# Performance work log

Hardware: AMD Instinct MI355X
Metric: run time of the kernel (lower is better)

The kernel has to match this reference:

```python
import jax, jax.numpy as jnp
import numpy as np

D = 512       # embed_dim
H = 8         # num_heads
HD = D // H   # head_dim = 64
B = 16
TQ = 512      # query length (current segment)
TK = 1024     # key length (memory + current)
GRU_BIAS = 2.0


def _layer_norm(x, g, b, eps=1e-5):
    mu = jnp.mean(x, axis=-1, keepdims=True)
    var = jnp.mean((x - mu) ** 2, axis=-1, keepdims=True)
    return (x - mu) * jax.lax.rsqrt(var + eps) * g + b


def _gelu(x):
    # torch nn.GELU() default is the exact erf form
    return jax.nn.gelu(x, approximate=False)


def _rel_shift(x):
    # Transformer-XL relative shift. x: [B, H, Tq, Tk]
    b, h, tq, tk = x.shape
    x = jnp.pad(x, ((0, 0), (0, 0), (0, 0), (1, 0)))
    x = x.reshape(b, h, tk + 1, tq)[:, :, 1:, :]
    return x.reshape(b, h, tq, tk)


def _gru_gate(x, y, W, bg):
    # GTrXL gating: x is the residual stream, y the sublayer output.
    Wr, Ur, Wz, Uz, Wg, Ug = W
    r = jax.nn.sigmoid(y @ Wr + x @ Ur)
    z = jax.nn.sigmoid(y @ Wz + x @ Uz - bg)
    h = jnp.tanh(y @ Wg + (r * x) @ Ug)
    return (1.0 - z) * x + z * h


def setup_inputs() -> dict:
    key = jax.random.key(0)
    ks = jax.random.split(key, 16)
    s = 0.02
    return {
        "query": jax.random.normal(ks[0], (B, TQ, D), jnp.float32),
        "key": jax.random.normal(ks[1], (B, TK, D), jnp.float32),
        "pos_embedding": jax.random.normal(ks[2], (TK, D), jnp.float32),
        "U": jax.random.normal(ks[3], (H, HD), jnp.float32) * s,
        "V": jax.random.normal(ks[4], (H, HD), jnp.float32) * s,
        # attention projections: Wq, Wk, Wv, Wpos, Wout (no biases)
        "attn_W": jax.random.normal(ks[5], (5, D, D), jnp.float32) * s,
        "ln1_g": jnp.ones((D,), jnp.float32),
        "ln1_b": jnp.zeros((D,), jnp.float32),
        "ln2_g": jnp.ones((D,), jnp.float32),
        "ln2_b": jnp.zeros((D,), jnp.float32),
        # GRU gates: stacked [Wr, Ur, Wz, Uz, Wg, Ug], bias bg init to gru_bias
        "gate1_W": jax.random.normal(ks[6], (6, D, D), jnp.float32) * s,
        "gate1_b": jnp.full((D,), GRU_BIAS, jnp.float32),
        "gate2_W": jax.random.normal(ks[7], (6, D, D), jnp.float32) * s,
        "gate2_b": jnp.full((D,), GRU_BIAS, jnp.float32),
        "fc_W1": jax.random.normal(ks[8], (D, 4 * D), jnp.float32) * s,
        "fc_b1": jnp.zeros((4 * D,), jnp.float32),
        "fc_W2": jax.random.normal(ks[9], (4 * D, D), jnp.float32) * s,
        "fc_b2": jnp.zeros((D,), jnp.float32),
    }


def reference(query, key, pos_embedding, U, V, attn_W,
              ln1_g, ln1_b, ln2_g, ln2_b,
              gate1_W, gate1_b, gate2_W, gate2_b,
              fc_W1, fc_b1, fc_W2, fc_b2):
    b, tq, d = query.shape
    tk = key.shape[1]
    hd = d // H

    nq = _layer_norm(query, ln1_g, ln1_b)
    nk = _layer_norm(key, ln1_g, ln1_b)

    Wq, Wk, Wv, Wp, Wo = attn_W
    q = (nq @ Wq).reshape(b, tq, H, hd)
    k = (nk @ Wk).reshape(b, tk, H, hd)
    v = (nk @ Wv).reshape(b, tk, H, hd)
    p = (pos_embedding @ Wp).reshape(tk, H, hd)

    # Transformer-XL: content score (q+U)k^T + position score (q+V)p^T (rel-shifted)
    AC = jnp.einsum('bqhd,bkhd->bhqk', q + U, k)
    BD = _rel_shift(jnp.einsum('bqhd,khd->bhqk', q + V, p))
    scores = (AC + BD) / jnp.sqrt(jnp.asarray(hd, query.dtype))
    attn = jax.nn.softmax(scores, axis=-1)

    Y = jnp.einsum('bhqk,bkhd->bqhd', attn, v).reshape(b, tq, d) @ Wo
    Y = _gelu(Y)  # dropout = 0.0

    out = _gru_gate(query, Y, gate1_W, gate1_b)
    h2 = _layer_norm(out, ln2_g, ln2_b)
    E = _gelu(_gelu(h2 @ fc_W1 + fc_b1) @ fc_W2 + fc_b2)
    out = _gru_gate(out, E, gate2_W, gate2_b)
    return out
```

## Files before the change

### kernel.cpp

```cpp
#include <hip/hip_runtime.h>
#include <hip/hip_bf16.h>

typedef unsigned short u16;
typedef __attribute__((ext_vector_type(4))) float f4;
typedef __attribute__((ext_vector_type(8))) short s16x8;
typedef __attribute__((ext_vector_type(8))) unsigned short u16x8;

__device__ __forceinline__ u16 f2bf(float x){
  unsigned u = __float_as_uint(x);
  u += 0x7fffu + ((u >> 16) & 1u);
  return (u16)(u >> 16);
}
__device__ __forceinline__ float bf2f(u16 h){ return __uint_as_float(((unsigned)h) << 16); }

__device__ __forceinline__ void gload_lds16(const u16* g, u16* l){
  __builtin_amdgcn_global_load_lds((__attribute__((address_space(1))) void*)g,
                                   (__attribute__((address_space(3))) void*)l, 16, 0, 0);
}

struct GemmP {
  const u16* A; const u16* B;
  const u16* A2; const u16* B2;
  int K1, K2, lda, ldb, H;
  long long sAb, sAh, sBb, sBh;
  u16* C; long long sCb, sCh; int ldc;
  u16* C2;
  const float* bias; const float* bias2;
  u16* S;
};

enum { EPI_BF16=0, EPI_QUV=1, EPI_SIG=2, EPI_TANH=3, EPI_GELU=4, EPI_BD=5 };

template<int BM, int BN, int EPI, int DB>
__launch_bounds__(256)
__global__ void gemm_k(GemmP p) {
  constexpr int WN = (BN >= 128) ? 2 : 1;
  constexpr int WM = 4 / WN;
  constexpr int TM = BM / WM, TN = BN / WN;
  constexpr int FM = TM / 16, FN = TN / 16;
  constexpr int BUFE = (BM + BN) * 64;

  __shared__ __align__(16) u16 lds[BUFE * (DB ? 2 : 1)];

  const int tid = threadIdx.x;
  const int w = tid >> 6, lane = tid & 63;
  const int bz = blockIdx.z;
  const int b = bz / p.H, h = bz - b * p.H;
  const int m0 = blockIdx.x * BM, n0 = blockIdx.y * BN;

  const u16* Ab0 = p.A + (long long)b * p.sAb + (long long)h * p.sAh + (long long)m0 * p.lda;
  const u16* Bb0 = p.B + (long long)b * p.sBb + (long long)h * p.sBh + (long long)n0 * p.ldb;
  const u16* Ab1 = p.A2 ? p.A2 + (long long)m0 * p.lda : (const u16*)0;
  const u16* Bb1 = p.B2 ? p.B2 + (long long)n0 * p.ldb : (const u16*)0;

  f4 acc[FM][FN];
  #pragma unroll
  for (int i = 0; i < FM; ++i)
    #pragma unroll
    for (int j = 0; j < FN; ++j) acc[i][j] = f4{0.f, 0.f, 0.f, 0.f};

  const int s1 = p.K1 >> 6;
  const int st = s1 + (p.K2 >> 6);
  const int wM = w / WN, wN = w - wM * WN;

  auto stage = [&](int s, u16* lA_, u16* lB_) {
    const u16* Ab; const u16* Bb; int k0;
    if (s < s1) { Ab = Ab0; Bb = Bb0; k0 = s << 6; }
    else        { Ab = Ab1; Bb = Bb1; k0 = (s - s1) << 6; }
    #pragma unroll
    for (int i = 0; i < (BM >> 5); ++i) {
      int c = i * 256 + tid, row = c >> 3, cc = c & 7, sc = cc ^ (row & 7);
      gload_lds16(Ab + (long long)row * p.lda + k0 + sc * 8, lA_ + (size_t)(i * 4 + w) * 512);
    }
    #pragma unroll
    for (int i = 0; i < (BN >> 5); ++i) {
      int c = i * 256 + tid, row = c >> 3, cc = c & 7, sc = cc ^ (row & 7);
      gload_lds16(Bb + (long long)row * p.ldb + k0 + sc * 8, lB_ + (size_t)(i * 4 + w) * 512);
    }
  };

  auto compute = [&](const u16* lA_, const u16* lB_) {
    #pragma unroll
    for (int kk = 0; kk < 2; ++kk) {
      const int kb = lane >> 4;
      const int gc = kk * 4 + kb;
      s16x8 av[FM], bv[FN];
      #pragma unroll
      for (int fm = 0; fm < FM; ++fm) {
        int r = wM * TM + fm * 16 + (lane & 15);
        av[fm] = *(const s16x8*)(lA_ + r * 64 + ((gc ^ (r & 7)) << 3));
      }
      #pragma unroll
      for (int fn = 0; fn < FN; ++fn) {
        int r = wN * TN + fn * 16 + (lane & 15);
        bv[fn] = *(const s16x8*)(lB_ + r * 64 + ((gc ^ (r & 7)) << 3));
      }
      #pragma unroll
      for (int fm = 0; fm < FM; ++fm)
        #pragma unroll
        for (int fn = 0; fn < FN; ++fn)
          acc[fm][fn] = __builtin_amdgcn_mfma_f32_16x16x32_bf16(av[fm], bv[fn], acc[fm][fn], 0, 0, 0);
    }
  };

  if constexpr (DB) {
    stage(0, lds, lds + BM * 64);
    __syncthreads();
    for (int s = 0; s < st; ++s) {
      u16* cur = lds + (size_t)(s & 1) * BUFE;
      if (s + 1 < st) {
        u16* nxt = lds + (size_t)((s + 1) & 1) * BUFE;
        stage(s + 1, nxt, nxt + BM * 64);
      }
      compute(cur, cur + BM * 64);
      __syncthreads();
    }
  } else {
    for (int s = 0; s < st; ++s) {
      stage(s, lds, lds + BM * 64);
      __syncthreads();
      compute(lds, lds + BM * 64);
      __syncthreads();
    }
  }

  const int rb = (lane >> 4) << 2;
  const int cb = lane & 15;

  if constexpr (EPI == EPI_BD) {
    #pragma unroll
    for (int fm = 0; fm < FM; ++fm)
      #pragma unroll
      for (int fn = 0; fn < FN; ++fn)
        #pragma unroll
        for (int r = 0; r < 4; ++r) {
          int row = m0 + wM * TM + fm * 16 + rb + r;
          int t   = n0 + wN * TN + fn * 16 + cb;
          int bb = row >> 9, q = row & 511;
          u16* Sp = p.S + (size_t)(bb * 8 + h) * 524800;
          Sp[(size_t)q * 1025 + 1 + t] = f2bf(acc[fm][fn][r] * 0.125f);
          if (t == 0 && q > 0) Sp[(size_t)q * 1025] = 0;
        }
  } else if constexpr (EPI == EPI_QUV) {
    #pragma unroll
    for (int fm = 0; fm < FM; ++fm)
      #pragma unroll
      for (int fn = 0; fn < FN; ++fn)
        #pragma unroll
        for (int r = 0; r < 4; ++r) {
          int row = m0 + wM * TM + fm * 16 + rb + r;
          int col = n0 + wN * TN + fn * 16 + cb;
          size_t o = (size_t)row * p.ldc + col;
          float x = acc[fm][fn][r];
          p.C[o]  = f2bf(x + p.bias[col]);
          p.C2[o] = f2bf(x + p.bias2[col]);
        }
  } else {
    u16* Cb = p.C + (long long)b * p.sCb + (long long)h * p.sCh;
    #pragma unroll
    for (int fm = 0; fm < FM; ++fm)
      #pragma unroll
      for (int fn = 0; fn < FN; ++fn)
        #pragma unroll
        for (int r = 0; r < 4; ++r) {
          int row = m0 + wM * TM + fm * 16 + rb + r;
          int col = n0 + wN * TN + fn * 16 + cb;
          float x = acc[fm][fn][r];
          if (p.bias) x += p.bias[col];
          if constexpr (EPI == EPI_SIG)  x = 1.f / (1.f + __expf(-x));
          if constexpr (EPI == EPI_TANH) { float e = __expf(-2.f * fabsf(x)); float t = (1.f - e) / (1.f + e); x = copysignf(t, x); }
          if constexpr (EPI == EPI_GELU) x = 0.5f * x * (1.f + erff(x * 0.70710678118654752f));
          Cb[(size_t)row * p.ldc + col] = f2bf(x);
        }
  }
}

__launch_bounds__(256)
__global__ void fattn_k(const u16* __restrict__ qU, const u16* __restrict__ kv,
                        const u16* __restrict__ vT, const u16* __restrict__ BD,
                        u16* __restrict__ Y) {
  __shared__ __align__(16) u16 sQ[128 * 64];
  __shared__ __align__(16) u16 sBuf[2 * 16384];

  const int tid = threadIdx.x, w = tid >> 6, lane = tid & 63;
  const int q0 = blockIdx.x * 128;
  const int bz = blockIdx.y, b = bz >> 3, h = bz & 7;
  const int cq = lane & 15, kb = lane >> 4;
  const u16* Sb = BD + (size_t)bz * 524800;

  auto stage = [&](int j0, u16* buf) {
    u16* sK_ = buf; u16* sV_ = buf + 4096; u16* sB_ = buf + 8192;
    #pragma unroll
    for (int i = 0; i < 2; ++i) {
      int c = i * 256 + tid, row = c >> 3, cc = c & 7, sc = cc ^ (row & 7);
      gload_lds16(kv + ((size_t)(b * 1024 + j0 + row)) * 1024 + h * 64 + sc * 8,
                  sK_ + (size_t)(i * 4 + w) * 512);
      gload_lds16(vT + (size_t)bz * 65536 + (size_t)row * 1024 + j0 + sc * 8,
                  sV_ + (size_t)(i * 4 + w) * 512);
    }
    #pragma unroll
    for (int i = 0; i < 4; ++i) {
      int c = i * 256 + tid, row = c >> 3, cc = c & 7, sc = cc ^ (row & 7);
      gload_lds16(Sb + 512 + (size_t)(q0 + row) * 1024 + j0 + sc * 8,
                  sB_ + (size_t)(i * 4 + w) * 512);
    }
  };

  #pragma unroll
  for (int i = 0; i < 4; ++i) {
    int c = i * 256 + tid, row = c >> 3, cc = c & 7, sc = cc ^ (row & 7);
    gload_lds16(qU + ((size_t)(b * 512 + q0 + row)) * 512 + h * 64 + sc * 8,
                sQ + (size_t)(i * 4 + w) * 512);
  }
  stage(0, sBuf);
  __syncthreads();

  float m_s[2][4], l_s[2][4];
  f4 O[2][4];
  #pragma unroll
  for (int fm = 0; fm < 2; ++fm)
    #pragma unroll
    for (int r = 0; r < 4; ++r) { m_s[fm][r] = -1e30f; l_s[fm][r] = 0.f; }
  #pragma unroll
  for (int fm = 0; fm < 2; ++fm)
    #pragma unroll
    for (int fd = 0; fd < 4; ++fd) O[fm][fd] = f4{0.f, 0.f, 0.f, 0.f};

  for (int it = 0; it < 16; ++it) {
    u16* buf = sBuf + (size_t)(it & 1) * 16384;
    u16* sK_ = buf; u16* sV_ = buf + 4096; u16* sPB_ = buf + 8192;
    if (it < 15) stage((it + 1) * 64, sBuf + (size_t)((it + 1) & 1) * 16384);

    f4 acc[2][4];
    #pragma unroll
    for (int fm = 0; fm < 2; ++fm)
      #pragma unroll
      for (int fn = 0; fn < 4; ++fn) acc[fm][fn] = f4{0.f, 0.f, 0.f, 0.f};
    #pragma unroll
    for (int kk = 0; kk < 2; ++kk) {
      int gc = kk * 4 + kb;
      s16x8 av[2], bv[4];
      #pragma unroll
      for (int fm = 0; fm < 2; ++fm) {
        int r = w * 32 + fm * 16 + cq;
        av[fm] = *(const s16x8*)(sQ + r * 64 + ((gc ^ (r & 7)) << 3));
      }
      #pragma unroll
      for (int fn = 0; fn < 4; ++fn) {
        int r = fn * 16 + cq;
        bv[fn] = *(const s16x8*)(sK_ + r * 64 + ((gc ^ (r & 7)) << 3));
      }
      #pragma unroll
      for (int fm = 0; fm < 2; ++fm)
        #pragma unroll
        for (int fn = 0; fn < 4; ++fn)
          acc[fm][fn] = __builtin_amdgcn_mfma_f32_16x16x32_bf16(av[fm], bv[fn], acc[fm][fn], 0, 0, 0);
    }

    float alr[2][4];
    #pragma unroll
    for (int fm = 0; fm < 2; ++fm) {
      #pragma unroll
      for (int r = 0; r < 4; ++r) {
        int row = w * 32 + fm * 16 + kb * 4 + r;
        int sw = row & 7;
        float sv[4];
        float tm = -1e30f;
        #pragma unroll
        for (int fn = 0; fn < 4; ++fn) {
          int j = fn * 16 + cq;
          float bd = bf2f(sPB_[row * 64 + (((j >> 3) ^ sw) << 3) + (j & 7)]);
          float s = acc[fm][fn][r] * 0.125f + bd;
          sv[fn] = s;
          tm = fmaxf(tm, s);
        }
        tm = fmaxf(tm, __shfl_xor(tm, 1));
        tm = fmaxf(tm, __shfl_xor(tm, 2));
        tm = fmaxf(tm, __shfl_xor(tm, 4));
        tm = fmaxf(tm, __shfl_xor(tm, 8));
        float mo = m_s[fm][r];
        float mn = fmaxf(mo, tm);
        float al = __expf(mo - mn);
        m_s[fm][r] = mn;
        float ps = 0.f;
        #pragma unroll
        for (int fn = 0; fn < 4; ++fn) {
          float pp = __expf(sv[fn] - mn);
          ps += pp;
          int j = fn * 16 + cq;
          sPB_[row * 64 + (((j >> 3) ^ sw) << 3) + (j & 7)] = f2bf(pp);
        }
        l_s[fm][r] = l_s[fm][r] * al + ps;
        alr[fm][r] = al;
      }
    }
    #pragma unroll
    for (int fm = 0; fm < 2; ++fm)
      #pragma unroll
      for (int fd = 0; fd < 4; ++fd)
        #pragma unroll
        for (int r = 0; r < 4; ++r) O[fm][fd][r] *= alr[fm][r];

    #pragma unroll
    for (int kk = 0; kk < 2; ++kk) {
      int m = kk * 4 + kb;
      s16x8 pa[2], vb[4];
      #pragma unroll
      for (int fm = 0; fm < 2; ++fm) {
        int r = w * 32 + fm * 16 + cq;
        pa[fm] = *(const s16x8*)(sPB_ + r * 64 + ((m ^ (r & 7)) << 3));
      }
      #pragma unroll
      for (int fd = 0; fd < 4; ++fd) {
        int rd = fd * 16 + cq;
        vb[fd] = *(const s16x8*)(sV_ + rd * 64 + ((m ^ (rd & 7)) << 3));
      }
      #pragma unroll
      for (int fm = 0; fm < 2; ++fm)
        #pragma unroll
        for (int fd = 0; fd < 4; ++fd)
          O[fm][fd] = __builtin_amdgcn_mfma_f32_16x16x32_bf16(pa[fm], vb[fd], O[fm][fd], 0, 0, 0);
    }
    __syncthreads();
  }

  #pragma unroll
  for (int fm = 0; fm < 2; ++fm)
    #pragma unroll
    for (int r = 0; r < 4; ++r) {
      float l = l_s[fm][r];
      l += __shfl_xor(l, 1); l += __shfl_xor(l, 2);
      l += __shfl_xor(l, 4); l += __shfl_xor(l, 8);
      l_s[fm][r] = 1.f / l;
    }
  #pragma unroll
  for (int fm = 0; fm < 2; ++fm)
    #pragma unroll
    for (int fd = 0; fd < 4; ++fd)
      #pragma unroll
      for (int r = 0; r < 4; ++r) {
        int row = q0 + w * 32 + fm * 16 + kb * 4 + r;
        int col = h * 64 + fd * 16 + cq;
        Y[(size_t)(b * 512 + row) * 512 + col] = f2bf(O[fm][fd][r] * l_s[fm][r]);
      }
}

__launch_bounds__(256)
__global__ void ln_k(const float* __restrict__ x, const float* __restrict__ g,
                     const float* __restrict__ be, u16* __restrict__ out) {
  int row  = blockIdx.x * 4 + (threadIdx.x >> 6);
  int lane = threadIdx.x & 63;
  const float* xr = x + (size_t)row * 512 + lane * 8;
  f4 v0 = *(const f4*)xr;
  f4 v1 = *(const f4*)(xr + 4);
  float s = 0.f, q = 0.f;
  #pragma unroll
  for (int i = 0; i < 4; ++i) { s += v0[i] + v1[i]; q += v0[i]*v0[i] + v1[i]*v1[i]; }
  #pragma unroll
  for (int o = 32; o > 0; o >>= 1) { s += __shfl_xor(s, o); q += __shfl_xor(q, o); }
  float mu = s * (1.f / 512.f);
  float rs = rsqrtf(q * (1.f / 512.f) - mu * mu + 1e-5f);
  int c = lane * 8;
  u16x8 o;
  #pragma unroll
  for (int i = 0; i < 8; ++i) {
    float xx = (i < 4) ? v0[i] : v1[i - 4];
    o[i] = f2bf((xx - mu) * rs * g[c + i] + be[c + i]);
  }
  *(u16x8*)(out + (size_t)row * 512 + c) = o;
}

__device__ __forceinline__ void tbody(float (*t)[65], const float* src, u16* dst,
                                      int R, int C, int bx, int by, int tid) {
  int c0 = bx * 64, r0 = by * 64;
  #pragma unroll
  for (int i = 0; i < 4; ++i) {
    int r = i * 16 + (tid >> 4);
    int c4 = (tid & 15) * 4;
    f4 v = *(const f4*)(src + (size_t)(r0 + r) * C + c0 + c4);
    t[r][c4] = v.x; t[r][c4 + 1] = v.y; t[r][c4 + 2] = v.z; t[r][c4 + 3] = v.w;
  }
  __syncthreads();
  #pragma unroll
  for (int i = 0; i < 2; ++i) {
    int id = i * 256 + tid;
    int rr = id >> 3, c8 = (id & 7) * 8;
    u16x8 o;
    #pragma unroll
    for (int j = 0; j < 8; ++j) o[j] = f2bf(t[c8 + j][rr]);
    *(u16x8*)(dst + (size_t)(c0 + rr) * R + r0 + c8) = o;
  }
}

__launch_bounds__(256)
__global__ void tsq_k(const float* aW, const float* g1W, const float* g2W, u16* wT) {
  __shared__ float t[64][65];
  int z = blockIdx.z;
  const int lut[6] = {0, 2, 1, 3, 4, 5};
  const float* src; u16* dst;
  if (z < 5)       { src = aW  + (size_t)z * 262144;        dst = wT + (size_t)z * 262144; }
  else if (z < 11) { int j = z - 5;  src = g1W + (size_t)j * 262144; dst = wT + (size_t)(5 + lut[j]) * 262144; }
  else             { int j = z - 11; src = g2W + (size_t)j * 262144; dst = wT + (size_t)(11 + lut[j]) * 262144; }
  tbody(t, src, dst, 512, 512, blockIdx.x, blockIdx.y, threadIdx.x);
}

__launch_bounds__(256)
__global__ void tgen_k(const float* src, u16* dst, int R, int C) {
  __shared__ float t[64][65];
  tbody(t, src, dst, R, C, blockIdx.x, blockIdx.y, threadIdx.x);
}

__launch_bounds__(256)
__global__ void vtrans_k(const u16* kv, u16* vT) {
  int jt = blockIdx.x, h = blockIdx.y, b = blockIdx.z;
  __shared__ u16 t[64][72];
  int tid = threadIdx.x;
  const u16* src = kv + ((size_t)b * 1024 + jt * 64) * 1024 + 512 + h * 64;
  #pragma unroll
  for (int i = 0; i < 2; ++i) {
    int id = i * 256 + tid;
    int r = id >> 3, c = (id & 7) * 8;
    u16x8 v = *(const u16x8*)(src + (size_t)r * 1024 + c);
    #pragma unroll
    for (int j = 0; j < 8; ++j) t[r][c + j] = v[j];
  }
  __syncthreads();
  u16* dst = vT + (size_t)(b * 8 + h) * 65536 + (size_t)jt * 64;
  #pragma unroll
  for (int i = 0; i < 2; ++i) {
    int id = i * 256 + tid;
    int d = id >> 3, c = (id & 7) * 8;
    u16x8 o;
    #pragma unroll
    for (int j = 0; j < 8; ++j) o[j] = t[c + j][d];
    *(u16x8*)(dst + (size_t)d * 1024 + c) = o;
  }
}

__launch_bounds__(256)
__global__ void conv_k(const float* in, u16* out, int n8) {
  int i = blockIdx.x * 256 + threadIdx.x;
  if (i >= n8) return;
  const float* p = in + (size_t)i * 8;
  f4 a = *(const f4*)p, b = *(const f4*)(p + 4);
  u16x8 o;
  #pragma unroll
  for (int j = 0; j < 4; ++j) { o[j] = f2bf(a[j]); o[4 + j] = f2bf(b[j]); }
  *(u16x8*)(out + (size_t)i * 8) = o;
}

__launch_bounds__(256)
__global__ void bias_k(const float* g1b, const float* g2b, float* b1, float* b2) {
  int i = blockIdx.x * 256 + threadIdx.x;
  if (i < 1024) { b1[i] = (i < 512) ? 0.f : -g1b[i - 512]; b2[i] = (i < 512) ? 0.f : -g2b[i - 512]; }
}

__launch_bounds__(256)
__global__ void rx_k(const u16* rz, const float* x, u16* rx) {
  int i = blockIdx.x * 256 + threadIdx.x;
  int m = i >> 6, d8 = (i & 63) << 3;
  u16x8 rv = *(const u16x8*)(rz + (size_t)m * 1024 + d8);
  const float* xp = x + (size_t)m * 512 + d8;
  f4 x0 = *(const f4*)xp, x1 = *(const f4*)(xp + 4);
  u16x8 o;
  #pragma unroll
  for (int j = 0; j < 4; ++j) { o[j] = f2bf(bf2f(rv[j]) * x0[j]); o[4 + j] = f2bf(bf2f(rv[4 + j]) * x1[j]); }
  *(u16x8*)(rx + (size_t)m * 512 + d8) = o;
}

__launch_bounds__(256)
__global__ void comb_k(const u16* rz, const u16* hg, const float* x, float* of, u16* ob) {
  int i = blockIdx.x * 256 + threadIdx.x;
  int m = i >> 6, d8 = (i & 63) << 3;
  u16x8 zv = *(const u16x8*)(rz + (size_t)m * 1024 + 512 + d8);
  u16x8 hv = *(const u16x8*)(hg + (size_t)m * 512 + d8);
  const float* xp = x + (size_t)m * 512 + d8;
  f4 x0 = *(const f4*)xp, x1 = *(const f4*)(xp + 4);
  f4 o0, o1; u16x8 obv;
  #pragma unroll
  for (int j = 0; j < 4; ++j) {
    float z = bf2f(zv[j]), hh = bf2f(hv[j]);
    float r = (1.f - z) * x0[j] + z * hh; o0[j] = r; obv[j] = f2bf(r);
  }
  #pragma unroll
  for (int j = 0; j < 4; ++j) {
    float z = bf2f(zv[4 + j]), hh = bf2f(hv[4 + j]);
    float r = (1.f - z) * x1[j] + z * hh; o1[j] = r; obv[4 + j] = f2bf(r);
  }
  float* op = of + (size_t)m * 512 + d8;
  *(f4*)op = o0; *(f4*)(op + 4) = o1;
  if (ob) *(u16x8*)(ob + (size_t)m * 512 + d8) = obv;
}

extern "C" void kernel_launch(void* const* d_in, const int* in_sizes, int n_in,
                              void* d_out, int out_size, void* d_ws, size_t ws_size,
                              hipStream_t stream) {
  const float* query = (const float*)d_in[0];
  const float* key   = (const float*)d_in[1];
  const float* pos   = (const float*)d_in[2];
  const float* U     = (const float*)d_in[3];
  const float* V     = (const float*)d_in[4];
  const float* attnW = (const float*)d_in[5];
  const float* ln1g  = (const float*)d_in[6];
  const float* ln1b  = (const float*)d_in[7];
  const float* ln2g  = (const float*)d_in[8];
  const float* ln2b  = (const float*)d_in[9];
  const float* g1W   = (const float*)d_in[10];
  const float* g1b   = (const float*)d_in[11];
  const float* g2W   = (const float*)d_in[12];
  const float* g2b   = (const float*)d_in[13];
  const float* fcW1  = (const float*)d_in[14];
  const float* fcb1  = (const float*)d_in[15];
  const float* fcW2  = (const float*)d_in[16];
  const float* fcb2  = (const float*)d_in[17];
  float* outp = (float*)d_out;

  char* base = (char*)d_ws;
  size_t off = 0;
  auto alloc = [&](size_t bytes) -> char* {
    char* p = base + off;
    off += (bytes + 255) & ~(size_t)255;
    return p;
  };

  u16* wT     = (u16*)alloc(17ull * 262144 * 2);
  u16* fc1T   = (u16*)alloc(2048ull * 512 * 2);
  u16* fc2T   = (u16*)alloc(2048ull * 512 * 2);
  u16* posb   = (u16*)alloc(1024ull * 512 * 2);
  u16* pbf    = (u16*)alloc(1024ull * 512 * 2);
  float* bias1 = (float*)alloc(1024 * 4);
  float* bias2 = (float*)alloc(1024 * 4);
  u16* nq     = (u16*)alloc(8192ull * 512 * 2);
  u16* nk     = (u16*)alloc(16384ull * 512 * 2);
  u16* xq     = (u16*)alloc(8192ull * 512 * 2);
  u16* qU     = (u16*)alloc(8192ull * 512 * 2);
  u16* qV     = (u16*)alloc(8192ull * 512 * 2);
  u16* kv     = (u16*)alloc(16384ull * 1024 * 2);
  u16* y1     = (u16*)alloc(8192ull * 512 * 2);
  u16* ob1    = (u16*)alloc(8192ull * 512 * 2);
  u16* S      = (u16*)alloc(128ull * 524800 * 2 + 4096);
  if (off > ws_size) return;

  u16* Y = nq;
  u16* vT = nk;
  float* out1f = (float*)qU;
  u16* rz1 = S;
  u16* rx1 = S + 8388608;
  u16* hg1 = rx1 + 4194304;
  u16* h2  = hg1 + 4194304;
  u16* e1  = h2 + 4194304;
  u16* y2  = e1 + 16777216;
  u16* rz2 = y2 + 4194304;
  u16* rx2 = rz2 + 8388608;
  u16* hg2 = rx2 + 4194304;

  bias_k<<<dim3(4), dim3(256), 0, stream>>>(g1b, g2b, bias1, bias2);
  tsq_k<<<dim3(8, 8, 17), dim3(256), 0, stream>>>(attnW, g1W, g2W, wT);
  tgen_k<<<dim3(32, 8), dim3(256), 0, stream>>>(fcW1, fc1T, 512, 2048);
  tgen_k<<<dim3(8, 32), dim3(256), 0, stream>>>(fcW2, fc2T, 2048, 512);
  conv_k<<<dim3(256), dim3(256), 0, stream>>>(pos, posb, 65536);
  conv_k<<<dim3(2048), dim3(256), 0, stream>>>(query, xq, 524288);
  ln_k<<<dim3(2048), dim3(256), 0, stream>>>(query, ln1g, ln1b, nq);
  ln_k<<<dim3(4096), dim3(256), 0, stream>>>(key, ln1g, ln1b, nk);

  { GemmP p{}; p.A = nq; p.B = wT; p.K1 = 512; p.lda = 512; p.ldb = 512; p.H = 1;
    p.C = qU; p.C2 = qV; p.ldc = 512; p.bias = U; p.bias2 = V;
    gemm_k<64,128,EPI_QUV,1><<<dim3(128,4,1), dim3(256), 0, stream>>>(p); }
  { GemmP p{}; p.A = nk; p.B = wT + 1ull*262144; p.K1 = 512; p.lda = 512; p.ldb = 512; p.H = 1;
    p.C = kv; p.ldc = 1024;
    gemm_k<128,128,EPI_BF16,0><<<dim3(128,8,1), dim3(256), 0, stream>>>(p); }
  { GemmP p{}; p.A = posb; p.B = wT + 3ull*262144; p.K1 = 512; p.lda = 512; p.ldb = 512; p.H = 1;
    p.C = pbf; p.ldc = 512;
    gemm_k<64,128,EPI_BF16,1><<<dim3(16,4,1), dim3(256), 0, stream>>>(p); }
  vtrans_k<<<dim3(16, 8, 16), dim3(256), 0, stream>>>(kv, vT);

  { GemmP p{}; p.A = qV; p.lda = 512; p.sAh = 64;
    p.B = pbf; p.ldb = 512; p.sBh = 64; p.K1 = 64; p.H = 8; p.S = S;
    gemm_k<128,128,EPI_BD,0><<<dim3(64,8,8), dim3(256), 0, stream>>>(p); }

  fattn_k<<<dim3(4, 128), dim3(256), 0, stream>>>(qU, kv, vT, S, Y);

  { GemmP p{}; p.A = Y; p.B = wT + 4ull*262144; p.K1 = 512; p.lda = 512; p.ldb = 512; p.H = 1;
    p.C = y1; p.ldc = 512;
    gemm_k<64,128,EPI_GELU,1><<<dim3(128,4,1), dim3(256), 0, stream>>>(p); }

  { GemmP p{}; p.A = y1; p.B = wT + 5ull*262144; p.K1 = 512;
    p.A2 = xq; p.B2 = wT + 7ull*262144; p.K2 = 512;
    p.lda = 512; p.ldb = 512; p.H = 1; p.C = rz1; p.ldc = 1024; p.bias = bias1;
    gemm_k<64,128,EPI_SIG,1><<<dim3(128,8,1), dim3(256), 0, stream>>>(p); }
  rx_k<<<dim3(2048), dim3(256), 0, stream>>>(rz1, query, rx1);
  { GemmP p{}; p.A = y1; p.B = wT + 9ull*262144; p.K1 = 512;
    p.A2 = rx1; p.B2 = wT + 10ull*262144; p.K2 = 512;
    p.lda = 512; p.ldb = 512; p.H = 1; p.C = hg1; p.ldc = 512;
    gemm_k<64,128,EPI_TANH,1><<<dim3(128,4,1), dim3(256), 0, stream>>>(p); }
  comb_k<<<dim3(2048), dim3(256), 0, stream>>>(rz1, hg1, query, out1f, ob1);

  ln_k<<<dim3(2048), dim3(256), 0, stream>>>(out1f, ln2g, ln2b, h2);
  { GemmP p{}; p.A = h2; p.B = fc1T; p.K1 = 512; p.lda = 512; p.ldb = 512; p.H = 1;
    p.C = e1; p.ldc = 2048; p.bias = fcb1;
    gemm_k<128,128,EPI_GELU,0><<<dim3(64,16,1), dim3(256), 0, stream>>>(p); }
  { GemmP p{}; p.A = e1; p.B = fc2T; p.K1 = 2048; p.lda = 2048; p.ldb = 2048; p.H = 1;
    p.C = y2; p.ldc = 512; p.bias = fcb2;
    gemm_k<64,128,EPI_GELU,1><<<dim3(128,4,1), dim3(256), 0, stream>>>(p); }

  { GemmP p{}; p.A = y2; p.B = wT + 11ull*262144; p.K1 = 512;
    p.A2 = ob1; p.B2 = wT + 13ull*262144; p.K2 = 512;
    p.lda = 512; p.ldb = 512; p.H = 1; p.C = rz2; p.ldc = 1024; p.bias = bias2;
    gemm_k<64,128,EPI_SIG,1><<<dim3(128,8,1), dim3(256), 0, stream>>>(p); }
  rx_k<<<dim3(2048), dim3(256), 0, stream>>>(rz2, out1f, rx2);
  { GemmP p{}; p.A = y2; p.B = wT + 15ull*262144; p.K1 = 512;
    p.A2 = rx2; p.B2 = wT + 16ull*262144; p.K2 = 512;
    p.lda = 512; p.ldb = 512; p.H = 1; p.C = hg2; p.ldc = 512;
    gemm_k<64,128,EPI_TANH,1><<<dim3(128,4,1), dim3(256), 0, stream>>>(p); }
  comb_k<<<dim3(2048), dim3(256), 0, stream>>>(rz2, hg2, out1f, outp, (u16*)nullptr);
}
```

Measured before the change: 448.1 us.

## Restructure flash attention to transposed S^T, register-resident Q and bpermute P

```diff
diff --git a/kernel.cpp b/kernel.cpp
--- a/kernel.cpp
+++ b/kernel.cpp
@@ -5,6 +5,9 @@
 typedef __attribute__((ext_vector_type(4))) float f4;
 typedef __attribute__((ext_vector_type(8))) short s16x8;
 typedef __attribute__((ext_vector_type(8))) unsigned short u16x8;
+typedef __attribute__((ext_vector_type(4))) unsigned short u16x4;
+typedef __attribute__((ext_vector_type(4))) int i32x4;
+typedef __attribute__((ext_vector_type(2))) unsigned u32x2;
 
 __device__ __forceinline__ u16 f2bf(float x){
   unsigned u = __float_as_uint(x);
@@ -12,6 +15,12 @@
   return (u16)(u >> 16);
 }
 __device__ __forceinline__ float bf2f(u16 h){ return __uint_as_float(((unsigned)h) << 16); }
+
+__device__ __forceinline__ unsigned cvt_pk_bf16(float lo, float hi){
+  unsigned r;
+  asm("v_cvt_pk_bf16_f32 %0, %1, %2" : "=v"(r) : "v"(lo), "v"(hi));
+  return r;
+}
 
 __device__ __forceinline__ void gload_lds16(const u16* g, u16* l){
   __builtin_amdgcn_global_load_lds((__attribute__((address_space(1))) void*)g,
@@ -175,11 +184,10 @@
   }
 }
 
-__launch_bounds__(256)
+__launch_bounds__(512)
 __global__ void fattn_k(const u16* __restrict__ qU, const u16* __restrict__ kv,
                         const u16* __restrict__ vT, const u16* __restrict__ BD,
                         u16* __restrict__ Y) {
-  __shared__ __align__(16) u16 sQ[128 * 64];
   __shared__ __align__(16) u16 sBuf[2 * 16384];
 
   const int tid = threadIdx.x, w = tid >> 6, lane = tid & 63;
@@ -190,159 +198,132 @@
 
   auto stage = [&](int j0, u16* buf) {
     u16* sK_ = buf; u16* sV_ = buf + 4096; u16* sB_ = buf + 8192;
+    {
+      int c = tid, row = c >> 3, cc = c & 7, sc = cc ^ (row & 7);
+      gload_lds16(kv + ((size_t)(b * 1024 + j0 + row)) * 1024 + h * 64 + sc * 8,
+                  sK_ + (size_t)w * 512);
+      gload_lds16(vT + (size_t)bz * 65536 + (size_t)row * 1024 + j0 + sc * 8,
+                  sV_ + (size_t)w * 512);
+    }
     #pragma unroll
     for (int i = 0; i < 2; ++i) {
-      int c = i * 256 + tid, row = c >> 3, cc = c & 7, sc = cc ^ (row & 7);
-      gload_lds16(kv + ((size_t)(b * 1024 + j0 + row)) * 1024 + h * 64 + sc * 8,
-                  sK_ + (size_t)(i * 4 + w) * 512);
-      gload_lds16(vT + (size_t)bz * 65536 + (size_t)row * 1024 + j0 + sc * 8,
-                  sV_ + (size_t)(i * 4 + w) * 512);
-    }
-    #pragma unroll
-    for (int i = 0; i < 4; ++i) {
-      int c = i * 256 + tid, row = c >> 3, cc = c & 7, sc = cc ^ (row & 7);
+      int c = i * 512 + tid, row = c >> 3, cc = c & 7, sc = cc ^ (row & 7);
       gload_lds16(Sb + 512 + (size_t)(q0 + row) * 1024 + j0 + sc * 8,
-                  sB_ + (size_t)(i * 4 + w) * 512);
+                  sB_ + (size_t)(i * 8 + w) * 512);
     }
   };
 
-  #pragma unroll
-  for (int i = 0; i < 4; ++i) {
-    int c = i * 256 + tid, row = c >> 3, cc = c & 7, sc = cc ^ (row & 7);
-    gload_lds16(qU + ((size_t)(b * 512 + q0 + row)) * 512 + h * 64 + sc * 8,
-                sQ + (size_t)(i * 4 + w) * 512);
-  }
+  const int qloc = w * 16 + cq;
+  const u16* qrow = qU + ((size_t)(b * 512 + q0 + qloc)) * 512 + h * 64;
+  s16x8 qb0 = *(const s16x8*)(qrow + kb * 8);
+  s16x8 qb1 = *(const s16x8*)(qrow + 32 + kb * 8);
+
   stage(0, sBuf);
   __syncthreads();
 
-  float m_s[2][4], l_s[2][4];
-  f4 O[2][4];
-  #pragma unroll
-  for (int fm = 0; fm < 2; ++fm)
-    #pragma unroll
-    for (int r = 0; r < 4; ++r) { m_s[fm][r] = -1e30f; l_s[fm][r] = 0.f; }
-  #pragma unroll
-  for (int fm = 0; fm < 2; ++fm)
-    #pragma unroll
-    for (int fd = 0; fd < 4; ++fd) O[fm][fd] = f4{0.f, 0.f, 0.f, 0.f};
+  float m_s = -1e30f, l_s = 0.f;
+  f4 O[4];
+  #pragma unroll
+  for (int fd = 0; fd < 4; ++fd) O[fd] = f4{0.f, 0.f, 0.f, 0.f};
+
+  const int sw = qloc & 7;
+  const int idxA = (cq + ((kb & 1) * 2) * 16) * 4;
+  const int idxB = idxA + 64;
 
   for (int it = 0; it < 16; ++it) {
     u16* buf = sBuf + (size_t)(it & 1) * 16384;
-    u16* sK_ = buf; u16* sV_ = buf + 4096; u16* sPB_ = buf + 8192;
+    u16* sK_ = buf; u16* sV_ = buf + 4096; u16* sB_ = buf + 8192;
     if (it < 15) stage((it + 1) * 64, sBuf + (size_t)((it + 1) & 1) * 16384);
 
-    f4 acc[2][4];
-    #pragma unroll
-    for (int fm = 0; fm < 2; ++fm)
-      #pragma unroll
-      for (int fn = 0; fn < 4; ++fn) acc[fm][fn] = f4{0.f, 0.f, 0.f, 0.f};
-    #pragma unroll
-    for (int kk = 0; kk < 2; ++kk) {
-      int gc = kk * 4 + kb;
-      s16x8 av[2], bv[4];
-      #pragma unroll
-      for (int fm = 0; fm < 2; ++fm) {
-        int r = w * 32 + fm * 16 + cq;
-        av[fm] = *(const s16x8*)(sQ + r * 64 + ((gc ^ (r & 7)) << 3));
+    f4 acc[4];
+    #pragma unroll
+    for (int fkv = 0; fkv < 4; ++fkv) acc[fkv] = f4{0.f, 0.f, 0.f, 0.f};
+    #pragma unroll
+    for (int fkv = 0; fkv < 4; ++fkv) {
+      int r = fkv * 16 + cq;
+      s16x8 a0 = *(const s16x8*)(sK_ + r * 64 + ((kb ^ (r & 7)) << 3));
+      s16x8 a1 = *(const s16x8*)(sK_ + r * 64 + (((4 + kb) ^ (r & 7)) << 3));
+      acc[fkv] = __builtin_amdgcn_mfma_f32_16x16x32_bf16(a0, qb0, acc[fkv], 0, 0, 0);
+      acc[fkv] = __builtin_amdgcn_mfma_f32_16x16x32_bf16(a1, qb1, acc[fkv], 0, 0, 0);
+    }
+
+    float p[4][4];
+    float tm = -1e30f;
+    #pragma unroll
+    for (int fkv = 0; fkv < 4; ++fkv) {
+      int j8 = 2 * fkv + (kb >> 1);
+      u16x4 bdv = *(const u16x4*)(sB_ + qloc * 64 + ((j8 ^ sw) << 3) + (kb & 1) * 4);
+      #pragma unroll
+      for (int r = 0; r < 4; ++r) {
+        float s = acc[fkv][r] * 0.125f + bf2f(bdv[r]);
+        p[fkv][r] = s;
+        tm = fmaxf(tm, s);
       }
-      #pragma unroll
-      for (int fn = 0; fn < 4; ++fn) {
-        int r = fn * 16 + cq;
-        bv[fn] = *(const s16x8*)(sK_ + r * 64 + ((gc ^ (r & 7)) << 3));
-      }
-      #pragma unroll
-      for (int fm = 0; fm < 2; ++fm)
-        #pragma unroll
-        for (int fn = 0; fn < 4; ++fn)
-          acc[fm][fn] = __builtin_amdgcn_mfma_f32_16x16x32_bf16(av[fm], bv[fn], acc[fm][fn], 0, 0, 0);
-    }
-
-    float alr[2][4];
-    #pragma unroll
-    for (int fm = 0; fm < 2; ++fm) {
-      #pragma unroll
-      for (int r = 0; r < 4; ++r) {
-        int row = w * 32 + fm * 16 + kb * 4 + r;
-        int sw = row & 7;
-        float sv[4];
-        float tm = -1e30f;
-        #pragma unroll
-        for (int fn = 0; fn < 4; ++fn) {
-          int j = fn * 16 + cq;
-          float bd = bf2f(sPB_[row * 64 + (((j >> 3) ^ sw) << 3) + (j & 7)]);
-          float s = acc[fm][fn][r] * 0.125f + bd;
-          sv[fn] = s;
-          tm = fmaxf(tm, s);
-        }
-        tm = fmaxf(tm, __shfl_xor(tm, 1));
-        tm = fmaxf(tm, __shfl_xor(tm, 2));
-        tm = fmaxf(tm, __shfl_xor(tm, 4));
-        tm = fmaxf(tm, __shfl_xor(tm, 8));
-        float mo = m_s[fm][r];
-        float mn = fmaxf(mo, tm);
-        float al = __expf(mo - mn);
-        m_s[fm][r] = mn;
-        float ps = 0.f;
-        #pragma unroll
-        for (int fn = 0; fn < 4; ++fn) {
-          float pp = __expf(sv[fn] - mn);
-          ps += pp;
-          int j = fn * 16 + cq;
-          sPB_[row * 64 + (((j >> 3) ^ sw) << 3) + (j & 7)] = f2bf(pp);
-        }
-        l_s[fm][r] = l_s[fm][r] * al + ps;
-        alr[fm][r] = al;
-      }
-    }
-    #pragma unroll
-    for (int fm = 0; fm < 2; ++fm)
-      #pragma unroll
-      for (int fd = 0; fd < 4; ++fd)
-        #pragma unroll
-        for (int r = 0; r < 4; ++r) O[fm][fd][r] *= alr[fm][r];
-
-    #pragma unroll
-    for (int kk = 0; kk < 2; ++kk) {
-      int m = kk * 4 + kb;
-      s16x8 pa[2], vb[4];
-      #pragma unroll
-      for (int fm = 0; fm < 2; ++fm) {
-        int r = w * 32 + fm * 16 + cq;
-        pa[fm] = *(const s16x8*)(sPB_ + r * 64 + ((m ^ (r & 7)) << 3));
-      }
+    }
+    tm = fmaxf(tm, __shfl_xor(tm, 16));
+    tm = fmaxf(tm, __shfl_xor(tm, 32));
+    float mn = fmaxf(m_s, tm);
+    float al = __expf(m_s - mn);
+    m_s = mn;
+    float ps = 0.f;
+    #pragma unroll
+    for (int fkv = 0; fkv < 4; ++fkv)
+      #pragma unroll
+      for (int r = 0; r < 4; ++r) { p[fkv][r] = __expf(p[fkv][r] - mn); ps += p[fkv][r]; }
+    ps += __shfl_xor(ps, 16);
+    ps += __shfl_xor(ps, 32);
+    l_s = l_s * al + ps;
+    #pragma unroll
+    for (int fd = 0; fd < 4; ++fd)
+      #pragma unroll
+      for (int r = 0; r < 4; ++r) O[fd][r] *= al;
+
+    unsigned W[4][2];
+    #pragma unroll
+    for (int fkv = 0; fkv < 4; ++fkv) {
+      W[fkv][0] = cvt_pk_bf16(p[fkv][0], p[fkv][1]);
+      W[fkv][1] = cvt_pk_bf16(p[fkv][2], p[fkv][3]);
+    }
+    s16x8 pb[2];
+    #pragma unroll
+    for (int c = 0; c < 2; ++c) {
+      int a00 = __builtin_amdgcn_ds_bpermute(idxA, (int)W[2 * c][0]);
+      int a01 = __builtin_amdgcn_ds_bpermute(idxA, (int)W[2 * c][1]);
+      int a10 = __builtin_amdgcn_ds_bpermute(idxA, (int)W[2 * c + 1][0]);
+      int a11 = __builtin_amdgcn_ds_bpermute(idxA, (int)W[2 * c + 1][1]);
+      int b00 = __builtin_amdgcn_ds_bpermute(idxB, (int)W[2 * c][0]);
+      int b01 = __builtin_amdgcn_ds_bpermute(idxB, (int)W[2 * c][1]);
+      int b10 = __builtin_amdgcn_ds_bpermute(idxB, (int)W[2 * c + 1][0]);
+      int b11 = __builtin_amdgcn_ds_bpermute(idxB, (int)W[2 * c + 1][1]);
+      bool hi = (kb >= 2);
+      i32x4 t;
+      t[0] = hi ? a10 : a00;
+      t[1] = hi ? a11 : a01;
+      t[2] = hi ? b10 : b00;
+      t[3] = hi ? b11 : b01;
+      pb[c] = *(s16x8*)&t;
+    }
+
+    #pragma unroll
+    for (int c = 0; c < 2; ++c)
       #pragma unroll
       for (int fd = 0; fd < 4; ++fd) {
         int rd = fd * 16 + cq;
-        vb[fd] = *(const s16x8*)(sV_ + rd * 64 + ((m ^ (rd & 7)) << 3));
+        s16x8 vb = *(const s16x8*)(sV_ + rd * 64 + (((c * 4 + kb) ^ (rd & 7)) << 3));
+        O[fd] = __builtin_amdgcn_mfma_f32_16x16x32_bf16(vb, pb[c], O[fd], 0, 0, 0);
       }
-      #pragma unroll
-      for (int fm = 0; fm < 2; ++fm)
-        #pragma unroll
-        for (int fd = 0; fd < 4; ++fd)
-          O[fm][fd] = __builtin_amdgcn_mfma_f32_16x16x32_bf16(pa[fm], vb[fd], O[fm][fd], 0, 0, 0);
-    }
     __syncthreads();
   }
 
-  #pragma unroll
-  for (int fm = 0; fm < 2; ++fm)
-    #pragma unroll
-    for (int r = 0; r < 4; ++r) {
-      float l = l_s[fm][r];
-      l += __shfl_xor(l, 1); l += __shfl_xor(l, 2);
-      l += __shfl_xor(l, 4); l += __shfl_xor(l, 8);
-      l_s[fm][r] = 1.f / l;
-    }
-  #pragma unroll
-  for (int fm = 0; fm < 2; ++fm)
-    #pragma unroll
-    for (int fd = 0; fd < 4; ++fd)
-      #pragma unroll
-      for (int r = 0; r < 4; ++r) {
-        int row = q0 + w * 32 + fm * 16 + kb * 4 + r;
-        int col = h * 64 + fd * 16 + cq;
-        Y[(size_t)(b * 512 + row) * 512 + col] = f2bf(O[fm][fd][r] * l_s[fm][r]);
-      }
+  float invl = 1.f / l_s;
+  u16* yrow = Y + ((size_t)(b * 512 + q0 + qloc)) * 512 + h * 64;
+  #pragma unroll
+  for (int fd = 0; fd < 4; ++fd) {
+    unsigned w0 = cvt_pk_bf16(O[fd][0] * invl, O[fd][1] * invl);
+    unsigned w1 = cvt_pk_bf16(O[fd][2] * invl, O[fd][3] * invl);
+    u32x2 st; st[0] = w0; st[1] = w1;
+    *(u32x2*)(yrow + fd * 16 + kb * 4) = st;
+  }
 }
 
 __launch_bounds__(256)
@@ -578,7 +559,7 @@
     p.B = pbf; p.ldb = 512; p.sBh = 64; p.K1 = 64; p.H = 8; p.S = S;
     gemm_k<128,128,EPI_BD,0><<<dim3(64,8,8), dim3(256), 0, stream>>>(p); }
 
-  fattn_k<<<dim3(4, 128), dim3(256), 0, stream>>>(qU, kv, vT, S, Y);
+  fattn_k<<<dim3(4, 128), dim3(512), 0, stream>>>(qU, kv, vT, S, Y);
 
   { GemmP p{}; p.A = Y; p.B = wT + 4ull*262144; p.K1 = 512; p.lda = 512; p.ldb = 512; p.H = 1;
     p.C = y1; p.ldc = 512;
```

Result: faster. 435.8 us (-2.7%).
